# Kernel optimization log

Measured on AMD Instinct MI355X. Metric: run time of the kernel, lower is better.

## Reference

```python
import jax, jax.numpy as jnp
import numpy as np

V, E, H, C, NC = 50000, 512, 512, 512, 2
B, T = 128, 512


def setup_inputs() -> dict:
    key = jax.random.key(0)
    ks = jax.random.split(key, 18)
    s = 0.05
    n = lambda k, shp: jax.random.normal(k, shp, dtype=jnp.float32) * s
    return {
        "tokens": jax.random.randint(ks[0], (B, T), 0, V, dtype=jnp.int32),
        "lengths": jax.random.randint(ks[1], (B,), T // 2, T + 1, dtype=jnp.int32),
        "emb": n(ks[2], (V, E)),
        "Wih_f": n(ks[3], (3 * H, E)), "Whh_f": n(ks[4], (3 * H, H)),
        "bih_f": n(ks[5], (3 * H,)), "bhh_f": n(ks[6], (3 * H,)),
        "Wih_b": n(ks[7], (3 * H, E)), "Whh_b": n(ks[8], (3 * H, H)),
        "bih_b": n(ks[9], (3 * H,)), "bhh_b": n(ks[10], (3 * H,)),
        "Wp": n(ks[11], (C, 2 * H)), "bp": n(ks[12], (C,)),
        "ctx": n(ks[13], (C,)),
        "Wl": n(ks[14], (NC, 2 * H)), "bl": n(ks[15], (NC,)),
    }


def _gru(x, mask, Wih, Whh, bih, bhh):
    """Unidirectional torch-style GRU. x:[B,T,E], mask:[B,T] -> [B,T,H].
    Hidden state is frozen on padded steps (pack_padded semantics)."""
    gi_all = jnp.swapaxes(x, 0, 1) @ Wih.T + bih  # [T,B,3H] input gates precomputed
    mT = jnp.swapaxes(mask, 0, 1)                 # [T,B]
    h0 = jnp.zeros((x.shape[0], Whh.shape[1]), x.dtype)

    def step(h, inp):
        gi, m = inp
        gh = h @ Whh.T + bhh
        ir, iz, i_n = jnp.split(gi, 3, axis=-1)
        hr, hz, h_n = jnp.split(gh, 3, axis=-1)
        r = jax.nn.sigmoid(ir + hr)
        z = jax.nn.sigmoid(iz + hz)
        nn_ = jnp.tanh(i_n + r * h_n)
        h_new = (1.0 - z) * nn_ + z * h
        h = jnp.where(m[:, None], h_new, h)
        return h, h

    _, out = jax.lax.scan(step, h0, (gi_all, mT))
    return jnp.swapaxes(out, 0, 1)


def _forward(tokens, lengths, emb, Wih_f, Whh_f, bih_f, bhh_f,
             Wih_b, Whh_b, bih_b, bhh_b, Wp, bp, ctx, Wl, bl):
    t_ar = jnp.arange(T)
    mask = t_ar[None, :] < lengths[:, None]          # [B,T] valid-token mask
    x = emb[tokens]                                   # [B,T,E]

    out_f = _gru(x, mask, Wih_f, Whh_f, bih_f, bhh_f)
    # reverse each sequence within its own length for the backward direction
    rev_idx = jnp.clip(lengths[:, None] - 1 - t_ar[None, :], 0, T - 1)  # [B,T]
    x_rev = jnp.take_along_axis(x, rev_idx[:, :, None], axis=1)
    out_b_rev = _gru(x_rev, mask, Wih_b, Whh_b, bih_b, bhh_b)
    out_b = jnp.take_along_axis(out_b_rev, rev_idx[:, :, None], axis=1)

    out = jnp.concatenate([out_f, out_b], axis=-1)    # [B,T,2H]
    out = out * mask[:, :, None].astype(out.dtype)    # zero pads (pad_packed_sequence)

    proj = jnp.tanh(out @ Wp.T + bp)                  # [B,T,C]
    scores = proj @ ctx                               # [B,T]
    scores = jnp.where(mask, scores, -jnp.inf)
    attn = jax.nn.softmax(scores, axis=1)             # masked softmax over valid words

    sent = jnp.einsum('bt,btd->bd', attn, out)        # attention pooling
    sent = jax.nn.selu(sent)                          # sentence_nonlinearity
    logits = sent @ Wl.T + bl                         # [B,NC]
    return logits, attn


def reference(tokens, lengths, emb, Wih_f, Whh_f, bih_f, bhh_f,
              Wih_b, Whh_b, bih_b, bhh_b, Wp, bp, ctx, Wl, bl):
    return _forward(tokens, lengths, emb, Wih_f, Whh_f, bih_f, bhh_f,
                    Wih_b, Whh_b, bih_b, bhh_b, Wp, bp, ctx, Wl, bl)
```

## Files before the change

kernel.cpp:

```cpp
#include <hip/hip_runtime.h>
#include <stdint.h>

#define B_  128
#define T_  512
#define H_  512
#define G3  1536

typedef __attribute__((ext_vector_type(8))) short bf16x8;
typedef __attribute__((ext_vector_type(4))) short bf16x4;
typedef __attribute__((ext_vector_type(4))) float f32x4;

#define MFMA16(a,b,c) __builtin_amdgcn_mfma_f32_16x16x32_bf16((a),(b),(c),0,0,0)

__device__ __forceinline__ unsigned short f2bf(float f) {
  union { float f; unsigned u; } v; v.f = f;
  unsigned r = v.u + 0x7FFFu + ((v.u >> 16) & 1u);
  return (unsigned short)(r >> 16);
}
__device__ __forceinline__ float bf2f(unsigned short u) {
  union { unsigned u; float f; } v; v.u = ((unsigned)u) << 16; return v.f;
}
__device__ __forceinline__ float sigm_f(float x) { return 1.f / (1.f + __expf(-x)); }
__device__ __forceinline__ float tanh_f(float x) { float e = __expf(2.f * x); return 1.f - 2.f / (e + 1.f); }

__launch_bounds__(256)
__global__ void k_cast(const float* __restrict__ Wih_f, const float* __restrict__ Wih_b,
                       const float* __restrict__ Whh_f, const float* __restrict__ Whh_b,
                       const float* __restrict__ Wp,
                       unsigned short* __restrict__ Wih, unsigned short* __restrict__ Whh,
                       unsigned short* __restrict__ Wpb, unsigned* __restrict__ flags) {
  int idx = blockIdx.x * 256 + threadIdx.x;
  if (idx < 65536) flags[idx] = 0;
  if (idx < 1572864) {
    float v = (idx < 786432) ? Wih_f[idx] : Wih_b[idx - 786432];
    Wih[idx] = f2bf(v);
  } else if (idx < 3145728) {
    int i2 = idx - 1572864;
    float v = (i2 < 786432) ? Whh_f[i2] : Whh_b[i2 - 786432];
    Whh[i2] = f2bf(v);
  } else if (idx < 3670016) {
    int i3 = idx - 3145728;
    Wpb[i3] = f2bf(Wp[i3]);
  }
}

__launch_bounds__(256)
__global__ void k_gather(const int* __restrict__ tokens, const float* __restrict__ emb,
                         unsigned short* __restrict__ xbf) {
  int row = blockIdx.x * 4 + (threadIdx.x >> 6);
  int lane = threadIdx.x & 63;
  int tok = tokens[row];
  const float4* src = (const float4*)(emb + (size_t)tok * 512);
  float4 v0 = src[lane * 2], v1 = src[lane * 2 + 1];
  bf16x8 pk;
  pk[0] = (short)f2bf(v0.x); pk[1] = (short)f2bf(v0.y);
  pk[2] = (short)f2bf(v0.z); pk[3] = (short)f2bf(v0.w);
  pk[4] = (short)f2bf(v1.x); pk[5] = (short)f2bf(v1.y);
  pk[6] = (short)f2bf(v1.z); pk[7] = (short)f2bf(v1.w);
  *(bf16x8*)&xbf[(size_t)row * 512 + lane * 8] = pk;
}

__launch_bounds__(256)
__global__ void k_igemm(const unsigned short* __restrict__ xbf,
                        const unsigned short* __restrict__ Wih,
                        float* __restrict__ gi) {
  __shared__ short smem[2 * 128 * 72];
  short* a_s = smem;
  short* b_s = smem + 128 * 72;
  int tid = threadIdx.x;
  int lane = tid & 63, w = tid >> 6;
  int quad = lane >> 4, l15 = lane & 15;
  int row0 = blockIdx.x * 128, col0 = blockIdx.y * 128;

  f32x4 acc[2][8];
  #pragma unroll
  for (int i = 0; i < 2; ++i)
    #pragma unroll
    for (int j = 0; j < 8; ++j) acc[i][j] = (f32x4){0.f, 0.f, 0.f, 0.f};

  for (int kt = 0; kt < 8; ++kt) {
    int k0 = kt * 64;
    __syncthreads();
    #pragma unroll
    for (int q = 0; q < 4; ++q) {
      int u = tid + 256 * q;
      int r = u >> 3, cu = u & 7;
      *(bf16x8*)&a_s[r * 72 + cu * 8] = *(const bf16x8*)&xbf[(size_t)(row0 + r) * 512 + k0 + cu * 8];
      *(bf16x8*)&b_s[r * 72 + cu * 8] = *(const bf16x8*)&Wih[(size_t)(col0 + r) * 512 + k0 + cu * 8];
    }
    __syncthreads();
    #pragma unroll
    for (int kk = 0; kk < 2; ++kk) {
      int kb = kk * 32 + quad * 8;
      bf16x8 a0 = *(const bf16x8*)&a_s[(w * 32 + l15) * 72 + kb];
      bf16x8 a1 = *(const bf16x8*)&a_s[(w * 32 + 16 + l15) * 72 + kb];
      #pragma unroll
      for (int nt = 0; nt < 8; ++nt) {
        bf16x8 bb = *(const bf16x8*)&b_s[(nt * 16 + l15) * 72 + kb];
        acc[0][nt] = MFMA16(a0, bb, acc[0][nt]);
        acc[1][nt] = MFMA16(a1, bb, acc[1][nt]);
      }
    }
  }

  int dir = col0 / 1536;
  int c2b = col0 - dir * 1536;
  int gate = c2b >> 9;
  int jjb = c2b & 511;
  size_t dbase = (size_t)dir * 65536ull * 1536ull;
  #pragma unroll
  for (int mt = 0; mt < 2; ++mt)
    #pragma unroll
    for (int nt = 0; nt < 8; ++nt) {
      int j5 = (jjb >> 4) + nt;
      #pragma unroll
      for (int r = 0; r < 4; ++r) {
        int row = row0 + 32 * w + 16 * mt + 4 * quad + r;
        gi[dbase + (size_t)row * 1536 + j5 * 48 + gate * 16 + l15] = acc[mt][nt][r];
      }
    }
}

__launch_bounds__(256, 1)
__global__ void k_rec2(const float* __restrict__ gi,
                       const unsigned short* __restrict__ Whh,
                       const float* __restrict__ bih_f, const float* __restrict__ bih_b,
                       const float* __restrict__ bhh_f, const float* __restrict__ bhh_b,
                       const int* __restrict__ lengths,
                       unsigned short* __restrict__ hbuf,
                       unsigned short* __restrict__ outb,
                       unsigned* __restrict__ flags) {
  __shared__ bf16x8 wlds[6][16][64];
  __shared__ unsigned short htile[4][256];
  __shared__ unsigned short otile[4][256];
  __shared__ int role_s[2];

  unsigned* ctrl = flags + 511 * 128;

  if (threadIdx.x == 0) {
    unsigned xcd;
    asm volatile("s_getreg_b32 %0, hwreg(HW_REG_XCC_ID)" : "=s"(xcd));
    xcd &= 7u;
    unsigned slot = atomicAdd(&ctrl[xcd], 1u);
    unsigned gv;
    if (slot == 0u) {
      gv = atomicAdd(&ctrl[8], 1u) + 1u;
      __hip_atomic_store(&ctrl[16u + xcd], gv, __ATOMIC_RELAXED, __HIP_MEMORY_SCOPE_AGENT);
    } else {
      do {
        gv = __hip_atomic_load(&ctrl[16u + xcd], __ATOMIC_RELAXED, __HIP_MEMORY_SCOPE_AGENT);
      } while (gv == 0u);
    }
    int gq = (int)gv - 1;
    role_s[0] = (gq < 4 && slot < 32u) ? gq : -1;
    role_s[1] = (int)(slot & 31u);
  }
  __syncthreads();
  int g = role_s[0];
  if (g < 0) return;
  int j5 = role_s[1];

  int tid = threadIdx.x;
  int lane = tid & 63, w = tid >> 6;
  int quad = lane >> 4, l15 = lane & 15;
  int dir = g >> 1, mh = g & 1;
  int j0 = j5 << 4;
  int jg = j0 + l15;
  int rb = mh * 64 + w * 16;

  const unsigned short* whh_g = Whh + (size_t)dir * (G3 * H_);
  const float* bih = dir ? bih_b : bih_f;
  const float* bhh = dir ? bhh_b : bhh_f;
  float b_r  = bih[jg] + bhh[jg];
  float b_z  = bih[512 + jg] + bhh[512 + jg];
  float b_in = bih[1024 + jg];
  float b_hn = bhh[1024 + jg];

  for (int wt = w; wt < 3; wt += 4) {
    const unsigned short* base =
        whh_g + (size_t)(wt * 512 + j0 + (lane & 15)) * 512;
    for (int s = 0; s < 16; ++s)
      wlds[wt][s][lane] = *(const bf16x8*)&base[s * 32 + (lane >> 4) * 8];
  }
  __syncthreads();

  int b0 = rb + l15;
  int Lg[4];
  #pragma unroll
  for (int r = 0; r < 4; ++r) Lg[r] = lengths[rb + 4 * quad + r];
  int bs = rb + (lane >> 2);
  int Ls = lengths[bs];
  int jp = lane & 3;

  unsigned short* hb = hbuf + (size_t)dir * (B_ * H_);
  float hreg[4] = {};

  size_t dbase = (size_t)dir * 65536ull * 1536ull;
  float gcur[12], gnxt[12];
  #pragma unroll
  for (int r = 0; r < 4; ++r) {
    int tx = dir ? (Lg[r] - 1) : 0;
    const float* gp = gi + dbase + ((size_t)(rb + 4 * quad + r) * T_ + tx) * 1536
                      + j5 * 48 + l15;
    gcur[3 * r + 0] = gp[0];
    gcur[3 * r + 1] = gp[16];
    gcur[3 * r + 2] = gp[32];
  }

  #pragma clang loop unroll(disable)
  for (int t = 0; t < T_; ++t) {
    const unsigned short* hc = hb + (size_t)(t & 1) * (2 * B_ * H_);
    unsigned short* hnx      = hb + (size_t)((t & 1) ^ 1) * (2 * B_ * H_);

    f32x4 acc_r = {0.f,0.f,0.f,0.f}, acc_z = {0.f,0.f,0.f,0.f};
    f32x4 acc_h = {0.f,0.f,0.f,0.f};

    if (t > 0) {
      if (w == 0 && lane < 32) {
        const unsigned* fp = &flags[(size_t)(t - 1) * 128 + g * 32 + lane];
        int spin = 0;
        unsigned v;
        do {
          asm volatile("global_load_dword %0, %1, off sc0\n\ts_waitcnt vmcnt(0)"
                       : "=v"(v) : "v"(fp) : "memory");
          if (v != 0u) break;
          asm volatile("s_sleep 1" ::: "memory");
        } while (++spin < (1 << 15));
      }
      __syncthreads();
      const unsigned short* hr0 = hc + (size_t)b0 * H_;
      bf16x8 ah[16];
      #pragma unroll
      for (int s = 0; s < 16; ++s) {
        asm volatile("global_load_dwordx4 %0, %1, off sc0"
                     : "=v"(ah[s]) : "v"(hr0 + s * 32 + quad * 8) : "memory");
      }
      asm volatile("s_waitcnt vmcnt(0)" ::: "memory");
      __builtin_amdgcn_sched_barrier(0);
      {
        int tn = (t + 1 < T_) ? (t + 1) : t;
        #pragma unroll
        for (int r = 0; r < 4; ++r) {
          int tx = dir ? ((tn < Lg[r]) ? (Lg[r] - 1 - tn) : 0) : tn;
          const float* gp = gi + dbase + ((size_t)(rb + 4 * quad + r) * T_ + tx) * 1536
                            + j5 * 48 + l15;
          gnxt[3 * r + 0] = gp[0];
          gnxt[3 * r + 1] = gp[16];
          gnxt[3 * r + 2] = gp[32];
        }
      }
      #pragma unroll
      for (int s = 0; s < 16; ++s) {
        acc_r = MFMA16(ah[s], wlds[0][s][lane], acc_r);
        acc_z = MFMA16(ah[s], wlds[1][s][lane], acc_z);
        acc_h = MFMA16(ah[s], wlds[2][s][lane], acc_h);
      }
    } else {
      int tn = 1;
      #pragma unroll
      for (int r = 0; r < 4; ++r) {
        int tx = dir ? ((tn < Lg[r]) ? (Lg[r] - 1 - tn) : 0) : tn;
        const float* gp = gi + dbase + ((size_t)(rb + 4 * quad + r) * T_ + tx) * 1536
                          + j5 * 48 + l15;
        gnxt[3 * r + 0] = gp[0];
        gnxt[3 * r + 1] = gp[16];
        gnxt[3 * r + 2] = gp[32];
      }
    }

    #pragma unroll
    for (int r = 0; r < 4; ++r) {
      int L = Lg[r];
      bool vld = t < L;
      float rr = sigm_f(acc_r[r] + gcur[3 * r + 0] + b_r);
      float zz = sigm_f(acc_z[r] + gcur[3 * r + 1] + b_z);
      float nn = tanh_f(gcur[3 * r + 2] + b_in + rr * (acc_h[r] + b_hn));
      float hold = hreg[r];
      float hnew = vld ? ((1.f - zz) * nn + zz * hold) : hold;
      hreg[r] = hnew;
      unsigned short hbf = f2bf(hnew);
      htile[w][(4 * quad + r) * 16 + l15] = hbf;
      otile[w][(4 * quad + r) * 16 + l15] = vld ? hbf : (unsigned short)0;
    }
    asm volatile("s_waitcnt lgkmcnt(0)" ::: "memory");
    unsigned long long hv = *(const unsigned long long*)&htile[w][(lane >> 2) * 16 + jp * 4];
    unsigned long long ov = *(const unsigned long long*)&otile[w][(lane >> 2) * 16 + jp * 4];
    asm volatile("global_store_dwordx2 %0, %1, off sc0"
                 :: "v"(&hnx[(size_t)bs * H_ + j0 + jp * 4]), "v"(hv) : "memory");
    bool vs = t < Ls;
    int p = dir ? (vs ? (Ls - 1 - t) : t) : t;
    *(unsigned long long*)&outb[((size_t)bs * T_ + p) * 1024 + dir * 512 + j0 + jp * 4] = ov;

    __syncthreads();
    if (tid == 0 && t < 511)
      asm volatile("global_store_dword %0, %1, off sc0"
                   :: "v"(&flags[(size_t)t * 128 + g * 32 + j5]), "v"(1u) : "memory");
    #pragma unroll
    for (int i = 0; i < 12; ++i) gcur[i] = gnxt[i];
  }
}

__launch_bounds__(256, 1)
__global__ void k_rec(const unsigned short* __restrict__ xbf,
                      const unsigned short* __restrict__ Wih,
                      const unsigned short* __restrict__ Whh,
                      const float* __restrict__ bih_f, const float* __restrict__ bih_b,
                      const float* __restrict__ bhh_f, const float* __restrict__ bhh_b,
                      const int* __restrict__ lengths,
                      unsigned short* __restrict__ hbuf,
                      unsigned short* __restrict__ outb,
                      unsigned* __restrict__ flags) {
  __shared__ bf16x8 wlds[6][16][64];
  __shared__ unsigned short htile[4][256];
  __shared__ unsigned short otile[4][256];
  __shared__ int role_s[2];

  unsigned* ctrl = flags + 511 * 128;

  if (threadIdx.x == 0) {
    unsigned xcd;
    asm volatile("s_getreg_b32 %0, hwreg(HW_REG_XCC_ID)" : "=s"(xcd));
    xcd &= 7u;
    unsigned slot = atomicAdd(&ctrl[xcd], 1u);
    unsigned gv;
    if (slot == 0u) {
      gv = atomicAdd(&ctrl[8], 1u) + 1u;
      __hip_atomic_store(&ctrl[16u + xcd], gv, __ATOMIC_RELAXED, __HIP_MEMORY_SCOPE_AGENT);
    } else {
      do {
        gv = __hip_atomic_load(&ctrl[16u + xcd], __ATOMIC_RELAXED, __HIP_MEMORY_SCOPE_AGENT);
      } while (gv == 0u);
    }
    int gq = (int)gv - 1;
    role_s[0] = (gq < 4 && slot < 32u) ? gq : -1;
    role_s[1] = (int)(slot & 31u);
  }
  __syncthreads();
  int g = role_s[0];
  if (g < 0) return;
  int j5 = role_s[1];

  int tid = threadIdx.x;
  int lane = tid & 63, w = tid >> 6;
  int quad = lane >> 4, l15 = lane & 15;
  int dir = g >> 1, mh = g & 1;
  int j0 = j5 << 4;
  int jg = j0 + l15;
  int rb = mh * 64 + w * 16;

  const unsigned short* wih_g = Wih + (size_t)dir * (G3 * H_);
  const unsigned short* whh_g = Whh + (size_t)dir * (G3 * H_);
  const float* bih = dir ? bih_b : bih_f;
  const float* bhh = dir ? bhh_b : bhh_f;
  float b_r  = bih[jg] + bhh[jg];
  float b_z  = bih[512 + jg] + bhh[512 + jg];
  float b_in = bih[1024 + jg];
  float b_hn = bhh[1024 + jg];

  for (int gi = w; gi < 6; gi += 4) {
    const unsigned short* base =
        (gi < 3 ? wih_g : whh_g) + (size_t)((gi % 3) * 512 + j0 + (lane & 15)) * 512;
    for (int s = 0; s < 16; ++s)
      wlds[gi][s][lane] = *(const bf16x8*)&base[s * 32 + (lane >> 4) * 8];
  }
  __syncthreads();

  int b0 = rb + l15;
  int L0 = lengths[b0];
  int Lg[4];
  #pragma unroll
  for (int r = 0; r < 4; ++r) Lg[r] = lengths[rb + 4 * quad + r];
  int bs = rb + (lane >> 2);
  int Ls = lengths[bs];
  int jp = lane & 3;

  unsigned short* hb = hbuf + (size_t)dir * (B_ * H_);
  float hreg[4] = {};

  bf16x8 ax[16];
  {
    int tx0 = dir ? (L0 - 1) : 0;
    const unsigned short* xr = xbf + ((size_t)b0 * T_ + tx0) * 512;
    #pragma unroll
    for (int s = 0; s < 16; ++s) ax[s] = *(const bf16x8*)&xr[s * 32 + quad * 8];
  }

  #pragma clang loop unroll(disable)
  for (int t = 0; t < T_; ++t) {
    const unsigned short* hc = hb + (size_t)(t & 1) * (2 * B_ * H_);
    unsigned short* hnx      = hb + (size_t)((t & 1) ^ 1) * (2 * B_ * H_);

    f32x4 acc_r = {0.f,0.f,0.f,0.f}, acc_z = {0.f,0.f,0.f,0.f};
    f32x4 acc_n = {0.f,0.f,0.f,0.f}, acc_h = {0.f,0.f,0.f,0.f};

    #pragma unroll
    for (int s = 0; s < 16; ++s) {
      acc_r = MFMA16(ax[s], wlds[0][s][lane], acc_r);
      acc_z = MFMA16(ax[s], wlds[1][s][lane], acc_z);
      acc_n = MFMA16(ax[s], wlds[2][s][lane], acc_n);
    }
    {
      int tn = (t + 1 < T_) ? (t + 1) : t;
      int tx1 = dir ? ((tn < L0) ? (L0 - 1 - tn) : 0) : tn;
      const unsigned short* xr1 = xbf + ((size_t)b0 * T_ + tx1) * 512;
      #pragma unroll
      for (int s = 0; s < 16; ++s) ax[s] = *(const bf16x8*)&xr1[s * 32 + quad * 8];
    }

    if (t > 0) {
      if (w == 0 && lane < 32) {
        const unsigned* fp = &flags[(size_t)(t - 1) * 128 + g * 32 + lane];
        int spin = 0;
        unsigned v;
        do {
          asm volatile("global_load_dword %0, %1, off sc0\n\ts_waitcnt vmcnt(0)"
                       : "=v"(v) : "v"(fp) : "memory");
          if (v != 0u) break;
          asm volatile("s_sleep 1" ::: "memory");
        } while (++spin < (1 << 15));
      }
      __syncthreads();
      const unsigned short* hr0 = hc + (size_t)b0 * H_;
      bf16x8 ah[16];
      #pragma unroll
      for (int s = 0; s < 16; ++s) {
        asm volatile("global_load_dwordx4 %0, %1, off sc0"
                     : "=v"(ah[s]) : "v"(hr0 + s * 32 + quad * 8) : "memory");
      }
      asm volatile("s_waitcnt vmcnt(0)" ::: "memory");
      __builtin_amdgcn_sched_barrier(0);
      #pragma unroll
      for (int s = 0; s < 16; ++s) {
        acc_r = MFMA16(ah[s], wlds[3][s][lane], acc_r);
        acc_z = MFMA16(ah[s], wlds[4][s][lane], acc_z);
        acc_h = MFMA16(ah[s], wlds[5][s][lane], acc_h);
      }
    }

    #pragma unroll
    for (int r = 0; r < 4; ++r) {
      int L = Lg[r];
      bool vld = t < L;
      float rr = sigm_f(acc_r[r] + b_r);
      float zz = sigm_f(acc_z[r] + b_z);
      float nn = tanh_f(acc_n[r] + b_in + rr * (acc_h[r] + b_hn));
      float hold = hreg[r];
      float hnew = vld ? ((1.f - zz) * nn + zz * hold) : hold;
      hreg[r] = hnew;
      unsigned short hbf = f2bf(hnew);
      htile[w][(4 * quad + r) * 16 + l15] = hbf;
      otile[w][(4 * quad + r) * 16 + l15] = vld ? hbf : (unsigned short)0;
    }
    asm volatile("s_waitcnt lgkmcnt(0)" ::: "memory");
    unsigned long long hv = *(const unsigned long long*)&htile[w][(lane >> 2) * 16 + jp * 4];
    unsigned long long ov = *(const unsigned long long*)&otile[w][(lane >> 2) * 16 + jp * 4];
    asm volatile("global_store_dwordx2 %0, %1, off sc0"
                 :: "v"(&hnx[(size_t)bs * H_ + j0 + jp * 4]), "v"(hv) : "memory");

    __syncthreads();
    if (tid == 0 && t < 511)
      asm volatile("global_store_dword %0, %1, off sc0"
                   :: "v"(&flags[(size_t)t * 128 + g * 32 + j5]), "v"(1u) : "memory");
    bool vs = t < Ls;
    int p = dir ? (vs ? (Ls - 1 - t) : t) : t;
    *(unsigned long long*)&outb[((size_t)bs * T_ + p) * 1024 + dir * 512 + j0 + jp * 4] = ov;
  }
}

__launch_bounds__(256)
__global__ void k_gemm2(const unsigned short* __restrict__ outbf,
                        const unsigned short* __restrict__ Wpb,
                        const float* __restrict__ bp, const float* __restrict__ ctx,
                        float* __restrict__ sc4) {
  __shared__ short smem[2 * 128 * 72];
  short* a_s = smem;
  short* b_s = smem + 128 * 72;
  int tid = threadIdx.x;
  int lane = tid & 63, w = tid >> 6;
  int quad = lane >> 4, l15 = lane & 15;
  int row0 = blockIdx.x * 128, col0 = blockIdx.y * 128;

  f32x4 acc[2][8];
  #pragma unroll
  for (int i = 0; i < 2; ++i)
    #pragma unroll
    for (int j = 0; j < 8; ++j) acc[i][j] = (f32x4){0.f, 0.f, 0.f, 0.f};

  for (int kt = 0; kt < 16; ++kt) {
    int k0 = kt * 64;
    __syncthreads();
    #pragma unroll
    for (int q = 0; q < 4; ++q) {
      int u = tid + 256 * q;
      int r = u >> 3, cu = u & 7;
      *(bf16x8*)&a_s[r * 72 + cu * 8] = *(const bf16x8*)&outbf[(size_t)(row0 + r) * 1024 + k0 + cu * 8];
      *(bf16x8*)&b_s[r * 72 + cu * 8] = *(const bf16x8*)&Wpb[(size_t)(col0 + r) * 1024 + k0 + cu * 8];
    }
    __syncthreads();
    #pragma unroll
    for (int kk = 0; kk < 2; ++kk) {
      int kb = kk * 32 + quad * 8;
      bf16x8 a0 = *(const bf16x8*)&a_s[(w * 32 + l15) * 72 + kb];
      bf16x8 a1 = *(const bf16x8*)&a_s[(w * 32 + 16 + l15) * 72 + kb];
      #pragma unroll
      for (int nt = 0; nt < 8; ++nt) {
        bf16x8 bb = *(const bf16x8*)&b_s[(nt * 16 + l15) * 72 + kb];
        acc[0][nt] = MFMA16(a0, bb, acc[0][nt]);
        acc[1][nt] = MFMA16(a1, bb, acc[1][nt]);
      }
    }
  }

  float rs[2][4] = {};
  #pragma unroll
  for (int mt = 0; mt < 2; ++mt) {
    #pragma unroll
    for (int nt = 0; nt < 8; ++nt) {
      int col = col0 + nt * 16 + l15;
      float bv = bp[col], cv = ctx[col];
      #pragma unroll
      for (int r = 0; r < 4; ++r) {
        float x = acc[mt][nt][r] + bv;
        rs[mt][r] += tanh_f(x) * cv;
      }
    }
  }
  #pragma unroll
  for (int mt = 0; mt < 2; ++mt) {
    #pragma unroll
    for (int r = 0; r < 4; ++r) {
      float v = rs[mt][r];
      v += __shfl_xor(v, 1); v += __shfl_xor(v, 2);
      v += __shfl_xor(v, 4); v += __shfl_xor(v, 8);
      if (l15 == 0)
        sc4[(size_t)blockIdx.y * 65536 + row0 + 32 * w + 16 * mt + 4 * quad + r] = v;
    }
  }
}

__launch_bounds__(64)
__global__ void k_softmax(const float* __restrict__ sc4, const int* __restrict__ lengths,
                          float* __restrict__ attn) {
  int b = blockIdx.x, lane = threadIdx.x;
  int L = lengths[b];
  float s[8]; float mx = -1e30f;
  #pragma unroll
  for (int i = 0; i < 8; ++i) {
    int t = lane + i * 64;
    int idx = b * T_ + t;
    float v = -1e30f;
    if (t < L)
      v = sc4[idx] + sc4[65536 + idx] + sc4[131072 + idx] + sc4[196608 + idx];
    s[i] = v;
    mx = fmaxf(mx, v);
  }
  #pragma unroll
  for (int o = 32; o; o >>= 1) mx = fmaxf(mx, __shfl_xor(mx, o));
  float sum = 0.f;
  #pragma unroll
  for (int i = 0; i < 8; ++i) {
    int t = lane + i * 64;
    s[i] = (t < L) ? __expf(s[i] - mx) : 0.f;
    sum += s[i];
  }
  #pragma unroll
  for (int o = 32; o; o >>= 1) sum += __shfl_xor(sum, o);
  float inv = 1.f / sum;
  #pragma unroll
  for (int i = 0; i < 8; ++i) attn[b * T_ + lane + i * 64] = s[i] * inv;
}

__launch_bounds__(256)
__global__ void k_final(const float* __restrict__ attn, const unsigned short* __restrict__ outb,
                        const int* __restrict__ lengths,
                        const float* __restrict__ Wl, const float* __restrict__ bl,
                        float* __restrict__ logits) {
  __shared__ float red[8];
  int b = blockIdx.x, tid = threadIdx.x;
  int L = lengths[b];
  float a0 = 0.f, a1 = 0.f, a2 = 0.f, a3 = 0.f;
  for (int t = 0; t < L; ++t) {
    float a = attn[b * T_ + t];
    const unsigned short* row = outb + ((size_t)b * T_ + t) * 1024 + tid * 4;
    bf16x4 v = *(const bf16x4*)row;
    a0 += a * bf2f((unsigned short)v[0]);
    a1 += a * bf2f((unsigned short)v[1]);
    a2 += a * bf2f((unsigned short)v[2]);
    a3 += a * bf2f((unsigned short)v[3]);
  }
  const float al = 1.6732632423543772f, sc = 1.0507009873554805f;
  float s0 = sc * (a0 > 0.f ? a0 : al * (__expf(a0) - 1.f));
  float s1 = sc * (a1 > 0.f ? a1 : al * (__expf(a1) - 1.f));
  float s2 = sc * (a2 > 0.f ? a2 : al * (__expf(a2) - 1.f));
  float s3 = sc * (a3 > 0.f ? a3 : al * (__expf(a3) - 1.f));
  int d = tid * 4;
  float p0 = s0 * Wl[d] + s1 * Wl[d + 1] + s2 * Wl[d + 2] + s3 * Wl[d + 3];
  float p1 = s0 * Wl[1024 + d] + s1 * Wl[1024 + d + 1] + s2 * Wl[1024 + d + 2] + s3 * Wl[1024 + d + 3];
  #pragma unroll
  for (int o = 32; o; o >>= 1) { p0 += __shfl_xor(p0, o); p1 += __shfl_xor(p1, o); }
  if ((tid & 63) == 0) { red[(tid >> 6) * 2] = p0; red[(tid >> 6) * 2 + 1] = p1; }
  __syncthreads();
  if (tid == 0) {
    logits[b * 2]     = red[0] + red[2] + red[4] + red[6] + bl[0];
    logits[b * 2 + 1] = red[1] + red[3] + red[5] + red[7] + bl[1];
  }
}

extern "C" void kernel_launch(void* const* d_in, const int* in_sizes, int n_in,
                              void* d_out, int out_size, void* d_ws, size_t ws_size,
                              hipStream_t stream) {
  const int*   tokens  = (const int*)d_in[0];
  const int*   lengths = (const int*)d_in[1];
  const float* emb     = (const float*)d_in[2];
  const float* Wih_f   = (const float*)d_in[3];
  const float* Whh_f   = (const float*)d_in[4];
  const float* bih_f   = (const float*)d_in[5];
  const float* bhh_f   = (const float*)d_in[6];
  const float* Wih_b   = (const float*)d_in[7];
  const float* Whh_b   = (const float*)d_in[8];
  const float* bih_b   = (const float*)d_in[9];
  const float* bhh_b   = (const float*)d_in[10];
  const float* Wp      = (const float*)d_in[11];
  const float* bp      = (const float*)d_in[12];
  const float* ctx     = (const float*)d_in[13];
  const float* Wl      = (const float*)d_in[14];
  const float* bl      = (const float*)d_in[15];
  float* out = (float*)d_out;

  char* ws = (char*)d_ws;
  unsigned short* Wih  = (unsigned short*)(ws + 0);
  unsigned short* Whh  = (unsigned short*)(ws + 3145728);
  unsigned short* Wpb  = (unsigned short*)(ws + 6291456);
  unsigned short* xbf  = (unsigned short*)(ws + 7340032);
  unsigned short* outb = (unsigned short*)(ws + 74448896);
  unsigned short* hbuf = (unsigned short*)(ws + 208666624);
  float* sc4           = (float*)(ws + 209190912);
  unsigned* flags      = (unsigned*)(ws + 210239488);
  const size_t GI_OFF  = 210501632ull;
  const size_t GI_SZ   = 805306368ull;
  float* gi            = (float*)(ws + GI_OFF);

  k_cast<<<14336, 256, 0, stream>>>(Wih_f, Wih_b, Whh_f, Whh_b, Wp, Wih, Whh, Wpb, flags);
  k_gather<<<16384, 256, 0, stream>>>(tokens, emb, xbf);
  if (ws_size >= GI_OFF + GI_SZ) {
    dim3 gg(512, 24);
    k_igemm<<<gg, 256, 0, stream>>>(xbf, Wih, gi);
    k_rec2<<<1024, 256, 0, stream>>>(gi, Whh, bih_f, bih_b, bhh_f, bhh_b,
                                     lengths, hbuf, outb, flags);
  } else {
    k_rec<<<1024, 256, 0, stream>>>(xbf, Wih, Whh, bih_f, bih_b, bhh_f, bhh_b,
                                    lengths, hbuf, outb, flags);
  }
  dim3 g2(512, 4);
  k_gemm2<<<g2, 256, 0, stream>>>(outb, Wpb, bp, ctx, sc4);
  k_softmax<<<128, 64, 0, stream>>>(sc4, lengths, out + 256);
  k_final<<<128, 256, 0, stream>>>(out + 256, outb, lengths, Wl, bl, out);
}
```

Measured before the change: 3.292 ms.

## Precompute input-gate projections per vocabulary entry and gather them in recurrence

Instead of gathering embeddings per token and computing a token-level input GEMM into a large fp32 gates buffer, the input projection is applied to the whole embedding table (50000 rows) once and stored in bf16. The recurrent kernel then fetches gate values by token id. This removes the gather kernel and halves the gate storage, but the GEMM now covers 50k rows instead of 65k tokens, and gate values are rounded to bf16, which adds precision error. The fallback path also moves the next-step x prefetch to after the hidden-state MFMAs.

```diff
diff --git a/kernel.cpp b/kernel.cpp
--- a/kernel.cpp
+++ b/kernel.cpp
@@ -5,6 +5,7 @@
 #define T_  512
 #define H_  512
 #define G3  1536
+#define EGR 50048ull
 
 typedef __attribute__((ext_vector_type(8))) short bf16x8;
 typedef __attribute__((ext_vector_type(4))) short bf16x4;
@@ -61,9 +62,9 @@
 }
 
 __launch_bounds__(256)
-__global__ void k_igemm(const unsigned short* __restrict__ xbf,
+__global__ void k_wgemm(const float* __restrict__ emb,
                         const unsigned short* __restrict__ Wih,
-                        float* __restrict__ gi) {
+                        unsigned short* __restrict__ eg) {
   __shared__ short smem[2 * 128 * 72];
   short* a_s = smem;
   short* b_s = smem + 128 * 72;
@@ -85,7 +86,15 @@
     for (int q = 0; q < 4; ++q) {
       int u = tid + 256 * q;
       int r = u >> 3, cu = u & 7;
-      *(bf16x8*)&a_s[r * 72 + cu * 8] = *(const bf16x8*)&xbf[(size_t)(row0 + r) * 512 + k0 + cu * 8];
+      int row = row0 + r; if (row >= 50000) row = 49999;
+      const float4* ap = (const float4*)(emb + (size_t)row * 512 + k0 + cu * 8);
+      float4 v0 = ap[0], v1 = ap[1];
+      bf16x8 pk;
+      pk[0] = (short)f2bf(v0.x); pk[1] = (short)f2bf(v0.y);
+      pk[2] = (short)f2bf(v0.z); pk[3] = (short)f2bf(v0.w);
+      pk[4] = (short)f2bf(v1.x); pk[5] = (short)f2bf(v1.y);
+      pk[6] = (short)f2bf(v1.z); pk[7] = (short)f2bf(v1.w);
+      *(bf16x8*)&a_s[r * 72 + cu * 8] = pk;
       *(bf16x8*)&b_s[r * 72 + cu * 8] = *(const bf16x8*)&Wih[(size_t)(col0 + r) * 512 + k0 + cu * 8];
     }
     __syncthreads();
@@ -107,7 +116,7 @@
   int c2b = col0 - dir * 1536;
   int gate = c2b >> 9;
   int jjb = c2b & 511;
-  size_t dbase = (size_t)dir * 65536ull * 1536ull;
+  size_t dbase = (size_t)dir * EGR * 1536ull;
   #pragma unroll
   for (int mt = 0; mt < 2; ++mt)
     #pragma unroll
@@ -116,20 +125,22 @@
       #pragma unroll
       for (int r = 0; r < 4; ++r) {
         int row = row0 + 32 * w + 16 * mt + 4 * quad + r;
-        gi[dbase + (size_t)row * 1536 + j5 * 48 + gate * 16 + l15] = acc[mt][nt][r];
+        if (row < 50000)
+          eg[dbase + (size_t)row * 1536 + j5 * 48 + gate * 16 + l15] = f2bf(acc[mt][nt][r]);
       }
     }
 }
 
 __launch_bounds__(256, 1)
-__global__ void k_rec2(const float* __restrict__ gi,
-                       const unsigned short* __restrict__ Whh,
-                       const float* __restrict__ bih_f, const float* __restrict__ bih_b,
-                       const float* __restrict__ bhh_f, const float* __restrict__ bhh_b,
-                       const int* __restrict__ lengths,
-                       unsigned short* __restrict__ hbuf,
-                       unsigned short* __restrict__ outb,
-                       unsigned* __restrict__ flags) {
+__global__ void k_rec2eg(const int* __restrict__ tokens,
+                         const unsigned short* __restrict__ eg,
+                         const unsigned short* __restrict__ Whh,
+                         const float* __restrict__ bih_f, const float* __restrict__ bih_b,
+                         const float* __restrict__ bhh_f, const float* __restrict__ bhh_b,
+                         const int* __restrict__ lengths,
+                         unsigned short* __restrict__ hbuf,
+                         unsigned short* __restrict__ outb,
+                         unsigned* __restrict__ flags) {
   __shared__ bf16x8 wlds[6][16][64];
   __shared__ unsigned short htile[4][256];
   __shared__ unsigned short otile[4][256];
@@ -186,8 +197,12 @@
 
   int b0 = rb + l15;
   int Lg[4];
-  #pragma unroll
-  for (int r = 0; r < 4; ++r) Lg[r] = lengths[rb + 4 * quad + r];
+  const int* trow[4];
+  #pragma unroll
+  for (int r = 0; r < 4; ++r) {
+    Lg[r] = lengths[rb + 4 * quad + r];
+    trow[r] = tokens + (size_t)(rb + 4 * quad + r) * T_;
+  }
   int bs = rb + (lane >> 2);
   int Ls = lengths[bs];
   int jp = lane & 3;
@@ -195,13 +210,12 @@
   unsigned short* hb = hbuf + (size_t)dir * (B_ * H_);
   float hreg[4] = {};
 
-  size_t dbase = (size_t)dir * 65536ull * 1536ull;
-  float gcur[12], gnxt[12];
+  const unsigned short* egd = eg + (size_t)dir * EGR * 1536ull + j5 * 48 + l15;
+  unsigned short gcur[12], gnxt[12];
   #pragma unroll
   for (int r = 0; r < 4; ++r) {
     int tx = dir ? (Lg[r] - 1) : 0;
-    const float* gp = gi + dbase + ((size_t)(rb + 4 * quad + r) * T_ + tx) * 1536
-                      + j5 * 48 + l15;
+    const unsigned short* gp = egd + (size_t)trow[r][tx] * 1536;
     gcur[3 * r + 0] = gp[0];
     gcur[3 * r + 1] = gp[16];
     gcur[3 * r + 2] = gp[32];
@@ -242,8 +256,7 @@
         #pragma unroll
         for (int r = 0; r < 4; ++r) {
           int tx = dir ? ((tn < Lg[r]) ? (Lg[r] - 1 - tn) : 0) : tn;
-          const float* gp = gi + dbase + ((size_t)(rb + 4 * quad + r) * T_ + tx) * 1536
-                            + j5 * 48 + l15;
+          const unsigned short* gp = egd + (size_t)trow[r][tx] * 1536;
           gnxt[3 * r + 0] = gp[0];
           gnxt[3 * r + 1] = gp[16];
           gnxt[3 * r + 2] = gp[32];
@@ -260,8 +273,7 @@
       #pragma unroll
       for (int r = 0; r < 4; ++r) {
         int tx = dir ? ((tn < Lg[r]) ? (Lg[r] - 1 - tn) : 0) : tn;
-        const float* gp = gi + dbase + ((size_t)(rb + 4 * quad + r) * T_ + tx) * 1536
-                          + j5 * 48 + l15;
+        const unsigned short* gp = egd + (size_t)trow[r][tx] * 1536;
         gnxt[3 * r + 0] = gp[0];
         gnxt[3 * r + 1] = gp[16];
         gnxt[3 * r + 2] = gp[32];
@@ -272,9 +284,9 @@
     for (int r = 0; r < 4; ++r) {
       int L = Lg[r];
       bool vld = t < L;
-      float rr = sigm_f(acc_r[r] + gcur[3 * r + 0] + b_r);
-      float zz = sigm_f(acc_z[r] + gcur[3 * r + 1] + b_z);
-      float nn = tanh_f(gcur[3 * r + 2] + b_in + rr * (acc_h[r] + b_hn));
+      float rr = sigm_f(acc_r[r] + bf2f(gcur[3 * r + 0]) + b_r);
+      float zz = sigm_f(acc_z[r] + bf2f(gcur[3 * r + 1]) + b_z);
+      float nn = tanh_f(bf2f(gcur[3 * r + 2]) + b_in + rr * (acc_h[r] + b_hn));
       float hold = hreg[r];
       float hnew = vld ? ((1.f - zz) * nn + zz * hold) : hold;
       hreg[r] = hnew;
@@ -399,13 +411,6 @@
       acc_z = MFMA16(ax[s], wlds[1][s][lane], acc_z);
       acc_n = MFMA16(ax[s], wlds[2][s][lane], acc_n);
     }
-    {
-      int tn = (t + 1 < T_) ? (t + 1) : t;
-      int tx1 = dir ? ((tn < L0) ? (L0 - 1 - tn) : 0) : tn;
-      const unsigned short* xr1 = xbf + ((size_t)b0 * T_ + tx1) * 512;
-      #pragma unroll
-      for (int s = 0; s < 16; ++s) ax[s] = *(const bf16x8*)&xr1[s * 32 + quad * 8];
-    }
 
     if (t > 0) {
       if (w == 0 && lane < 32) {
@@ -435,6 +440,14 @@
         acc_z = MFMA16(ah[s], wlds[4][s][lane], acc_z);
         acc_h = MFMA16(ah[s], wlds[5][s][lane], acc_h);
       }
+    }
+
+    {
+      int tn = (t + 1 < T_) ? (t + 1) : t;
+      int tx1 = dir ? ((tn < L0) ? (L0 - 1 - tn) : 0) : tn;
+      const unsigned short* xr1 = xbf + ((size_t)b0 * T_ + tx1) * 512;
+      #pragma unroll
+      for (int s = 0; s < 16; ++s) ax[s] = *(const bf16x8*)&xr1[s * 32 + quad * 8];
     }
 
     #pragma unroll
@@ -631,28 +644,44 @@
   unsigned short* Wih  = (unsigned short*)(ws + 0);
   unsigned short* Whh  = (unsigned short*)(ws + 3145728);
   unsigned short* Wpb  = (unsigned short*)(ws + 6291456);
-  unsigned short* xbf  = (unsigned short*)(ws + 7340032);
-  unsigned short* outb = (unsigned short*)(ws + 74448896);
-  unsigned short* hbuf = (unsigned short*)(ws + 208666624);
-  float* sc4           = (float*)(ws + 209190912);
-  unsigned* flags      = (unsigned*)(ws + 210239488);
-  const size_t GI_OFF  = 210501632ull;
-  const size_t GI_SZ   = 805306368ull;
-  float* gi            = (float*)(ws + GI_OFF);
-
-  k_cast<<<14336, 256, 0, stream>>>(Wih_f, Wih_b, Whh_f, Whh_b, Wp, Wih, Whh, Wpb, flags);
-  k_gather<<<16384, 256, 0, stream>>>(tokens, emb, xbf);
-  if (ws_size >= GI_OFF + GI_SZ) {
-    dim3 gg(512, 24);
-    k_igemm<<<gg, 256, 0, stream>>>(xbf, Wih, gi);
-    k_rec2<<<1024, 256, 0, stream>>>(gi, Whh, bih_f, bih_b, bhh_f, bhh_b,
-                                     lengths, hbuf, outb, flags);
+
+  const size_t EG_OFF    = 7340032ull;
+  const size_t EG_SZ     = 2ull * EGR * 1536ull * 2ull;
+  const size_t OUTB_A    = EG_OFF + EG_SZ;
+  const size_t HBUF_A    = OUTB_A + 134217728ull;
+  const size_t SC4_A     = HBUF_A + 524288ull;
+  const size_t FLAGS_A   = SC4_A + 1048576ull;
+  const size_t NEED_A    = FLAGS_A + 262144ull;
+
+  unsigned short* xbf   = (unsigned short*)(ws + 7340032);
+  unsigned short* outbB = (unsigned short*)(ws + 74448896);
+  unsigned short* hbufB = (unsigned short*)(ws + 208666624);
+  float* sc4B           = (float*)(ws + 209190912);
+  unsigned* flagsB      = (unsigned*)(ws + 210239488);
+
+  if (ws_size >= NEED_A) {
+    unsigned short* eg    = (unsigned short*)(ws + EG_OFF);
+    unsigned short* outbA = (unsigned short*)(ws + OUTB_A);
+    unsigned short* hbufA = (unsigned short*)(ws + HBUF_A);
+    float* sc4A           = (float*)(ws + SC4_A);
+    unsigned* flagsA      = (unsigned*)(ws + FLAGS_A);
+    k_cast<<<14336, 256, 0, stream>>>(Wih_f, Wih_b, Whh_f, Whh_b, Wp, Wih, Whh, Wpb, flagsA);
+    dim3 gw(391, 24);
+    k_wgemm<<<gw, 256, 0, stream>>>(emb, Wih, eg);
+    k_rec2eg<<<1024, 256, 0, stream>>>(tokens, eg, Whh, bih_f, bih_b, bhh_f, bhh_b,
+                                       lengths, hbufA, outbA, flagsA);
+    dim3 g2(512, 4);
+    k_gemm2<<<g2, 256, 0, stream>>>(outbA, Wpb, bp, ctx, sc4A);
+    k_softmax<<<128, 64, 0, stream>>>(sc4A, lengths, out + 256);
+    k_final<<<128, 256, 0, stream>>>(out + 256, outbA, lengths, Wl, bl, out);
   } else {
+    k_cast<<<14336, 256, 0, stream>>>(Wih_f, Wih_b, Whh_f, Whh_b, Wp, Wih, Whh, Wpb, flagsB);
+    k_gather<<<16384, 256, 0, stream>>>(tokens, emb, xbf);
     k_rec<<<1024, 256, 0, stream>>>(xbf, Wih, Whh, bih_f, bih_b, bhh_f, bhh_b,
-                                    lengths, hbuf, outb, flags);
-  }
-  dim3 g2(512, 4);
-  k_gemm2<<<g2, 256, 0, stream>>>(outb, Wpb, bp, ctx, sc4);
-  k_softmax<<<128, 64, 0, stream>>>(sc4, lengths, out + 256);
-  k_final<<<128, 256, 0, stream>>>(out + 256, outb, lengths, Wl, bl, out);
-}
+                                    lengths, hbufB, outbB, flagsB);
+    dim3 g2(512, 4);
+    k_gemm2<<<g2, 256, 0, stream>>>(outbB, Wpb, bp, ctx, sc4B);
+    k_softmax<<<128, 64, 0, stream>>>(sc4B, lengths, out + 256);
+    k_final<<<128, 256, 0, stream>>>(out + 256, outbB, lengths, Wl, bl, out);
+  }
+}
```

Result: slower. 9.502 ms (+188.7%).
